# Optimization experiments

Hardware: AMD Instinct MI355X
Metric: run time of the kernel (lower is better)

Reference implementation:

```python
import jax, jax.numpy as jnp
import numpy as np

B, S, D = 4, 8192, 512
WS = 512        # window_size
LB = 1          # look_backward (look_forward = 0, causal)


def setup_inputs() -> dict:
    key = jax.random.key(0)
    k1, k2, k3 = jax.random.split(key, 3)
    text = jax.random.normal(k1, (B, S, D), dtype=jnp.float32)
    audio = jax.random.normal(k2, (B, S, D), dtype=jnp.float32)
    video = jax.random.normal(k3, (B, S, D), dtype=jnp.float32)
    return {"text": text, "audio": audio, "video": video}


def _local_attention(q, k, v, ws=WS, lb=LB):
    # q, k, v: [b, n, d]; sliding-window causal attention, each query window
    # attends to its own window plus `lb` previous windows.
    b, n, d = q.shape
    w = n // ws
    scale = d ** -0.5
    qw = q.reshape(b, w, ws, d) * scale
    kw = k.reshape(b, w, ws, d)
    vw = v.reshape(b, w, ws, d)

    def look_around(x):
        # pad lb windows of zeros at the front, gather lb+1 shifted views
        padded = jnp.pad(x, ((0, 0), (lb, 0), (0, 0), (0, 0)))
        return jnp.concatenate([padded[:, i:i + w] for i in range(lb + 1)], axis=2)

    kk = look_around(kw)  # [b, w, (lb+1)*ws, d]
    vv = look_around(vw)

    # absolute positions for causal + padding mask
    t = jnp.arange(n).reshape(w, ws)                        # query positions [w, ws]
    tk = jnp.pad(t, ((lb, 0), (0, 0)), constant_values=-1)  # pad windows get -1
    bq_k = jnp.concatenate([tk[i:i + w] for i in range(lb + 1)], axis=1)  # [w, (lb+1)*ws]
    mask = (t[:, :, None] >= bq_k[:, None, :]) & (bq_k[:, None, :] >= 0)  # [w, ws, (lb+1)*ws]

    sim = jnp.einsum('bwid,bwjd->bwij', qw, kk)             # [b, w, ws, (lb+1)*ws]
    sim = jnp.where(mask[None], sim, jnp.finfo(sim.dtype).min)
    attn = jax.nn.softmax(sim, axis=-1)
    out = jnp.einsum('bwij,bwjd->bwid', attn, vv)
    return out.reshape(b, n, d)


def reference(text, audio, video):
    # GATSBlock.forward: x = self.local_attn(text, audio, video)
    # i.e. q = text, k = audio, v = video (modalities pre-projected to [b, n, d])
    return _local_attention(text, audio, video)
```

## Files before the change

### kernel.cpp

```cpp
#include <hip/hip_runtime.h>
#include <hip/hip_bf16.h>

#define S_ 8192
#define D_ 512
#define WSZ 512
#define QBLK 128
#define KBLK 64
#define ATT_THREADS 512
#define PPSTRIDE 4352
#define ATT_LDS (131072 + 4 * PPSTRIDE)

using bf16x8 = __attribute__((ext_vector_type(8))) __bf16;
using f32x4  = __attribute__((ext_vector_type(4))) float;
using f32x16 = __attribute__((ext_vector_type(16))) float;

#define GLDS(gp, lp) __builtin_amdgcn_global_load_lds( \
    (const __attribute__((address_space(1))) void*)(gp), \
    (__attribute__((address_space(3))) void*)(lp), 16, 0, 0)

__global__ __launch_bounds__(256) void cvt_k(const float* __restrict__ in,
                                             ushort* __restrict__ out) {
    const int bid = blockIdx.x;
    const int j = bid & 7, t = (bid >> 3) & 255, b = bid >> 11;
    const int u = j * 256 + threadIdx.x;
    const int c = u >> 7, row = (u >> 2) & 31, h = u & 3;
    const float* src = in + ((size_t)(b * S_ + t * 32 + row)) * D_ + c * 32 + h * 8;
    float4 a0 = *(const float4*)(src);
    float4 a1 = *(const float4*)(src + 4);
    bf16x8 o;
    o[0] = (__bf16)a0.x; o[1] = (__bf16)a0.y; o[2] = (__bf16)a0.z; o[3] = (__bf16)a0.w;
    o[4] = (__bf16)a1.x; o[5] = (__bf16)a1.y; o[6] = (__bf16)a1.z; o[7] = (__bf16)a1.w;
    *(bf16x8*)(out + (size_t)(b * 256 + t) * 16384 + u * 8) = o;
}

__global__ __launch_bounds__(256) void tr_v(const float* __restrict__ V,
                                            char* __restrict__ Vt) {
    __shared__ float tile[64][68];
    const int bid = blockIdx.x;
    const int d0 = (bid & 7) * 64;
    const int s0 = ((bid >> 3) & 127) * 64;
    const int b  = bid >> 10;
    const int t  = threadIdx.x;
    {
        const int sl = t >> 2, cg = (t & 3) * 16;
        const float* src = V + ((size_t)b * S_ + s0 + sl) * D_ + d0 + cg;
        #pragma unroll
        for (int j = 0; j < 4; ++j)
            *(float4*)&tile[sl][cg + j * 4] = *(const float4*)(src + j * 4);
    }
    __syncthreads();
    {
        const int dl = t >> 2, sg = (t & 3) * 16;
        const int d  = d0 + dl;
        const int tt = (s0 + sg) >> 5;
        const int kk = (s0 + sg) & 31;
        bf16x8 o0, o1;
        #pragma unroll
        for (int j = 0; j < 8; ++j) {
            o0[j] = (__bf16)tile[sg + j][dl];
            o1[j] = (__bf16)tile[sg + 8 + j][dl];
        }
        char* base = Vt + (size_t)(b * 256 + tt) * 32768 +
                     (d >> 5) * 2048 + (d & 31) * 16;
        *(bf16x8*)(base + (kk >> 4) * 1024)       = o0;
        *(bf16x8*)(base + (kk >> 4) * 1024 + 512) = o1;
    }
}

__global__ __launch_bounds__(ATT_THREADS, 2) void gats_attn(
    const float* __restrict__ Qg, const char* __restrict__ Kbg,
    const char* __restrict__ Vtg, float* __restrict__ Og)
{
    extern __shared__ char smem[];
    char* Vsh = smem + 65536;
    const int tid  = threadIdx.x;
    const int lane = tid & 63;
    const int wv   = tid >> 6;
    const int h    = lane >> 4;
    const int lq   = lane & 15;
    const int hh   = lane >> 5;
    const int l31  = lane & 31;
    const int u    = wv & 1;
    const int pr   = wv >> 1;
    char* Pp = smem + 131072 + pr * PPSTRIDE;
    char* Pf = Pp + 4096;
    const int laneK = lq * 64 + h * 16;

    const int bid = blockIdx.x;
    const int r2  = bid >> 3;
    const int w   = (bid & 7) * 2 + (r2 & 1);
    const int b   = (r2 >> 1) & 3;
    const int y   = r2 >> 3;
    const int qbase    = w * WSZ + y * QBLK;
    const int pairbase = qbase + pr * 32;
    const int wqbase   = qbase + wv * 16;

    const float* Qp  = Qg  + (size_t)b * S_ * D_;
    const char*  Kbp = Kbg + (size_t)b * 256 * 32768;
    const char*  Vtp = Vtg + (size_t)b * 256 * 32768;
    float*       Op  = Og  + (size_t)b * S_ * D_;

    const float scale = 0.044194173824159216f;
    const float L2E   = 1.44269504088896f;

    bf16x8 qf[16];
    {
        const int qrow = wqbase + lq;
        const float* qsrc = Qp + (size_t)qrow * D_ + h * 8;
        #pragma unroll
        for (int c = 0; c < 16; ++c) {
            float4 a0 = *(const float4*)(qsrc + c * 32);
            float4 a1 = *(const float4*)(qsrc + c * 32 + 4);
            bf16x8 q;
            q[0] = (__bf16)(a0.x * scale); q[1] = (__bf16)(a0.y * scale);
            q[2] = (__bf16)(a0.z * scale); q[3] = (__bf16)(a0.w * scale);
            q[4] = (__bf16)(a1.x * scale); q[5] = (__bf16)(a1.y * scale);
            q[6] = (__bf16)(a1.z * scale); q[7] = (__bf16)(a1.w * scale);
            qf[c] = q;
        }
    }

    f32x16 acc[8];
    #pragma unroll
    for (int dt = 0; dt < 8; ++dt)
        #pragma unroll
        for (int rg = 0; rg < 16; ++rg) acc[dt][rg] = 0.f;
    float m_run = -1e30f, l_run = 0.f;

    const int kstart = (w == 0) ? 0 : (w - 1) * WSZ;
    const int ktend  = qbase + QBLK;

    auto STAGE_K = [&](int kt) {
        const char* ksrc = Kbp + (((size_t)(kt >> 5)) << 15);
        #pragma unroll
        for (int s2 = 0; s2 < 8; ++s2) {
            const int off = wv * 8192 + s2 * 1024;
            GLDS(ksrc + off + lane * 16, smem + off);
        }
    };
    auto STAGE_V = [&](int kt) {
        const char* vsrc = Vtp + (((size_t)(kt >> 5)) << 15);
        #pragma unroll
        for (int s2 = 0; s2 < 8; ++s2) {
            const int off = wv * 8192 + s2 * 1024;
            GLDS(vsrc + off + lane * 16, Vsh + off);
        }
    };

    STAGE_K(kstart);
    STAGE_V(kstart);
    for (int kt = kstart; kt < ktend; kt += KBLK) {
        asm volatile("s_waitcnt vmcnt(0)" ::: "memory");
        __builtin_amdgcn_s_barrier();

        const bool act = (kt <= pairbase + 31);
        f32x4 st[4];

        if (act) {
            __builtin_amdgcn_s_setprio(1);
            #pragma unroll
            for (int g = 0; g < 4; ++g) {
                f32x4 sa = (f32x4){0.f, 0.f, 0.f, 0.f};
                f32x4 sb = (f32x4){0.f, 0.f, 0.f, 0.f};
                #pragma unroll
                for (int c = 0; c < 16; ++c) {
                    const int byte = (g >> 1) * 32768 + c * 2048 + (g & 1) * 1024 + laneK;
                    bf16x8 kf = *(const bf16x8*)(smem + byte);
                    if (c & 1) sb = __builtin_amdgcn_mfma_f32_16x16x32_bf16(kf, qf[c], sb, 0, 0, 0);
                    else       sa = __builtin_amdgcn_mfma_f32_16x16x32_bf16(kf, qf[c], sa, 0, 0, 0);
                }
                st[g] = sa + sb;
            }
            __builtin_amdgcn_s_setprio(0);

            const int qg = wqbase + lq;
            if (kt + 63 > wqbase) {
                #pragma unroll
                for (int g = 0; g < 4; ++g)
                    #pragma unroll
                    for (int r = 0; r < 4; ++r) {
                        const int key = kt + g * 16 + h * 4 + r;
                        if (key > qg) st[g][r] = -1e30f;
                    }
            }

            float own = -1e30f;
            #pragma unroll
            for (int g = 0; g < 4; ++g)
                #pragma unroll
                for (int r = 0; r < 4; ++r) own = fmaxf(own, st[g][r]);
            float tmax = fmaxf(own, __shfl_xor(own, 16));
            tmax = fmaxf(tmax, __shfl_xor(tmax, 32));

            const bool anyneed = __any(tmax > m_run + 8.f);
            float f_val = 1.0f;
            if (anyneed) {
                const float mnew = fmaxf(m_run, tmax);
                f_val = exp2f((m_run - mnew) * L2E);
                m_run = mnew;
                l_run *= f_val;
            }

            float p[4][4];
            float rs = 0.f;
            #pragma unroll
            for (int g = 0; g < 4; ++g)
                #pragma unroll
                for (int r = 0; r < 4; ++r) {
                    const float v = exp2f((st[g][r] - m_run) * L2E);
                    p[g][r] = v;
                    rs += v;
                }
            rs += __shfl_xor(rs, 16);
            rs += __shfl_xor(rs, 32);
            l_run += rs;

            uint cA[4], cB[4];
            #pragma unroll
            for (int g = 0; g < 4; ++g) {
                asm("v_cvt_pk_bf16_f32 %0, %1, %2" : "=v"(cA[g]) : "v"(p[g][0]), "v"(p[g][1]));
                asm("v_cvt_pk_bf16_f32 %0, %1, %2" : "=v"(cB[g]) : "v"(p[g][2]), "v"(p[g][3]));
            }
            const int wbase = (h >> 1) * 512 + (h & 1) * 8 + (u * 16 + lq) * 16;
            #pragma unroll
            for (int g = 0; g < 4; ++g) {
                *(uint*)(Pp + g * 1024 + wbase)     = cA[g];
                *(uint*)(Pp + g * 1024 + wbase + 4) = cB[g];
            }
            if (h == 0)    *(float*)(Pf + (u * 16 + lq) * 4) = f_val;
            if (lane == 0) *(uint*)(Pf + 128 + u * 4) = anyneed ? 1u : 0u;
        }

        asm volatile("s_waitcnt lgkmcnt(0)" ::: "memory");
        __builtin_amdgcn_sched_barrier(0);
        __builtin_amdgcn_s_barrier();

        if (kt + KBLK < ktend) STAGE_K(kt + KBLK);

        if (act) {
            const uint2 fl = *(const uint2*)(Pf + 128);
            if (fl.x | fl.y) {
                f32x4 fr[4];
                #pragma unroll
                for (int i = 0; i < 4; ++i)
                    fr[i] = *(const f32x4*)(Pf + i * 32 + hh * 16);
                #pragma unroll
                for (int dt = 0; dt < 8; ++dt)
                    #pragma unroll
                    for (int rg = 0; rg < 16; ++rg)
                        acc[dt][rg] *= fr[rg >> 2][rg & 3];
            }

            bf16x8 pa[4];
            #pragma unroll
            for (int ks = 0; ks < 4; ++ks)
                pa[ks] = *(const bf16x8*)(Pp + ks * 1024 + hh * 512 + l31 * 16);
            __builtin_amdgcn_s_setprio(1);
            #pragma unroll
            for (int dt = 0; dt < 8; ++dt) {
                #pragma unroll
                for (int ks = 0; ks < 4; ++ks) {
                    const int vb = (ks >> 1) * 32768 + (u * 8 + dt) * 2048 +
                                   (ks & 1) * 1024 + hh * 512 + l31 * 16;
                    bf16x8 vf = *(const bf16x8*)(Vsh + vb);
                    acc[dt] = __builtin_amdgcn_mfma_f32_32x32x16_bf16(pa[ks], vf, acc[dt], 0, 0, 0);
                }
            }
            __builtin_amdgcn_s_setprio(0);
        }
        __builtin_amdgcn_s_barrier();
        if (kt + KBLK < ktend) STAGE_V(kt + KBLK);
    }

    if (h == 0) *(float*)(Pf + (u * 16 + lq) * 4) = l_run;
    asm volatile("s_waitcnt lgkmcnt(0)" ::: "memory");
    __builtin_amdgcn_s_barrier();
    f32x4 iv[4];
    #pragma unroll
    for (int i = 0; i < 4; ++i) {
        f32x4 lv = *(const f32x4*)(Pf + i * 32 + hh * 16);
        iv[i][0] = 1.0f / lv[0]; iv[i][1] = 1.0f / lv[1];
        iv[i][2] = 1.0f / lv[2]; iv[i][3] = 1.0f / lv[3];
    }
    #pragma unroll
    for (int dt = 0; dt < 8; ++dt) {
        const int colb = u * 256 + dt * 32 + l31;
        #pragma unroll
        for (int rg = 0; rg < 16; ++rg) {
            const int row = pairbase + (rg & 3) + 8 * (rg >> 2) + 4 * hh;
            Op[(size_t)row * D_ + colb] = acc[dt][rg] * iv[rg >> 2][rg & 3];
        }
    }
}

#define FB_LDS (32768 + 32768 + 4 * 1024)
__global__ __launch_bounds__(256, 2) void gats_attn_fb(
    const float* __restrict__ Qg, const float* __restrict__ Kg,
    const float* __restrict__ Vg, float* __restrict__ Og)
{
    extern __shared__ char smem[];
    char* Ksh = smem;
    char* Vsh = smem + 32768;
    const int tid  = threadIdx.x;
    const int lane = tid & 63;
    const int wv   = tid >> 6;
    char* Psh = smem + 65536 + wv * 1024;
    const int bid = blockIdx.x;
    const int wh  = bid & 7;
    const int r2  = bid >> 3;
    const int w   = wh * 2 + (r2 & 1);
    const int b   = (r2 >> 1) & 3;
    const int y   = r2 >> 3;
    const int qbase  = w * WSZ + y * 64;
    const int wqbase = qbase + wv * 16;
    const size_t boff = (size_t)b * S_ * D_;
    const float* Qp = Qg + boff; const float* Kp = Kg + boff;
    const float* Vp = Vg + boff; float* Op = Og + boff;
    const float scale = 0.044194173824159216f;
    const float L2E   = 1.44269504088896f;
    bf16x8 qf[16];
    {
        const int qrow = wqbase + (lane & 15);
        const float* qsrc = Qp + (size_t)qrow * D_ + ((lane >> 4) * 8);
        #pragma unroll
        for (int c = 0; c < 16; ++c) {
            float4 a0 = *(const float4*)(qsrc + c * 32);
            float4 a1 = *(const float4*)(qsrc + c * 32 + 4);
            bf16x8 q;
            q[0] = (__bf16)(a0.x * scale); q[1] = (__bf16)(a0.y * scale);
            q[2] = (__bf16)(a0.z * scale); q[3] = (__bf16)(a0.w * scale);
            q[4] = (__bf16)(a1.x * scale); q[5] = (__bf16)(a1.y * scale);
            q[6] = (__bf16)(a1.z * scale); q[7] = (__bf16)(a1.w * scale);
            qf[c] = q;
        }
    }
    f32x4 acc[32];
    #pragma unroll
    for (int i = 0; i < 32; ++i) acc[i] = (f32x4){0.f, 0.f, 0.f, 0.f};
    float m_r[4], l_r[4];
    #pragma unroll
    for (int r = 0; r < 4; ++r) { m_r[r] = -1e30f; l_r[r] = 0.f; }
    const int kstart = (w == 0) ? 0 : (w - 1) * WSZ;
    const int ktend  = qbase + 64;
    for (int kt = kstart; kt < ktend; kt += 32) {
        __syncthreads();
        #pragma unroll
        for (int s = 0; s < 8; ++s) {
            const int row = s * 4 + wv;
            const int dof = lane * 8;
            const float4* src = (const float4*)(Kp + (size_t)(kt + row) * D_ + dof);
            float4 a0 = src[0], a1 = src[1];
            bf16x8 kv;
            kv[0] = (__bf16)a0.x; kv[1] = (__bf16)a0.y; kv[2] = (__bf16)a0.z; kv[3] = (__bf16)a0.w;
            kv[4] = (__bf16)a1.x; kv[5] = (__bf16)a1.y; kv[6] = (__bf16)a1.z; kv[7] = (__bf16)a1.w;
            const int byte = row * 1024 + ((dof * 2) ^ ((row & 7) << 4));
            *(bf16x8*)(Ksh + byte) = kv;
        }
        #pragma unroll
        for (int hh2 = 0; hh2 < 2; ++hh2) {
            const int d = tid + hh2 * 256;
            #pragma unroll
            for (int it = 0; it < 4; ++it) {
                float vvv[8];
                #pragma unroll
                for (int j = 0; j < 8; ++j)
                    vvv[j] = Vp[(size_t)(kt + it * 8 + j) * D_ + d];
                bf16x8 vb;
                #pragma unroll
                for (int j = 0; j < 8; ++j) vb[j] = (__bf16)vvv[j];
                const int byte = d * 64 + ((it * 16) ^ (((d >> 1) & 3) << 4));
                *(bf16x8*)(Vsh + byte) = vb;
            }
        }
        __syncthreads();
        if (kt > wqbase + 15) continue;
        f32x4 sacc[2];
        #pragma unroll
        for (int g = 0; g < 2; ++g) {
            f32x4 s = (f32x4){0.f, 0.f, 0.f, 0.f};
            const int keyrow = g * 16 + (lane & 15);
            #pragma unroll
            for (int c = 0; c < 16; ++c) {
                const int byte = keyrow * 1024 +
                                 ((c * 64 + (lane >> 4) * 16) ^ ((keyrow & 7) << 4));
                bf16x8 kf = *(const bf16x8*)(Ksh + byte);
                s = __builtin_amdgcn_mfma_f32_16x16x32_bf16(qf[c], kf, s, 0, 0, 0);
            }
            sacc[g] = s;
        }
        #pragma unroll
        for (int g = 0; g < 2; ++g) {
            if (kt + g * 16 + 15 > wqbase) {
                const int kg = kt + g * 16 + (lane & 15);
                #pragma unroll
                for (int r = 0; r < 4; ++r) {
                    const int qrow = wqbase + (lane >> 4) * 4 + r;
                    if (kg > qrow) sacc[g][r] = -1e30f;
                }
            }
        }
        float tmax[4];
        #pragma unroll
        for (int r = 0; r < 4; ++r) {
            float v = fmaxf(sacc[0][r], sacc[1][r]);
            #pragma unroll
            for (int off = 8; off >= 1; off >>= 1)
                v = fmaxf(v, __shfl_xor(v, off));
            tmax[r] = v;
        }
        bool need = false;
        #pragma unroll
        for (int r = 0; r < 4; ++r) need |= (tmax[r] > m_r[r] + 8.f);
        if (__any(need)) {
            #pragma unroll
            for (int r = 0; r < 4; ++r) {
                const float mnew = fmaxf(m_r[r], tmax[r]);
                const float f = exp2f((m_r[r] - mnew) * L2E);
                m_r[r] = mnew; l_r[r] *= f;
                #pragma unroll
                for (int dc = 0; dc < 32; ++dc) acc[dc][r] *= f;
            }
        }
        float rsum[4] = {0.f, 0.f, 0.f, 0.f};
        #pragma unroll
        for (int g = 0; g < 2; ++g) {
            #pragma unroll
            for (int r = 0; r < 4; ++r) {
                const float p = exp2f((sacc[g][r] - m_r[r]) * L2E);
                rsum[r] += p;
                const int prow = (lane >> 4) * 4 + r;
                const int byte = prow * 64 +
                                 ((g * 32 + (lane & 15) * 2) ^ (((prow >> 1) & 3) << 4));
                *(__bf16*)(Psh + byte) = (__bf16)p;
            }
        }
        #pragma unroll
        for (int r = 0; r < 4; ++r) {
            float v = rsum[r];
            #pragma unroll
            for (int off = 8; off >= 1; off >>= 1)
                v += __shfl_xor(v, off);
            l_r[r] += v;
        }
        {
            const int prow  = lane & 15;
            const int pbyte = prow * 64 +
                              (((lane >> 4) * 16) ^ (((prow >> 1) & 3) << 4));
            bf16x8 pa = *(const bf16x8*)(Psh + pbyte);
            #pragma unroll
            for (int dc = 0; dc < 32; ++dc) {
                const int d = dc * 16 + (lane & 15);
                const int vbyte = d * 64 +
                                  (((lane >> 4) * 16) ^ (((d >> 1) & 3) << 4));
                bf16x8 vf = *(const bf16x8*)(Vsh + vbyte);
                acc[dc] = __builtin_amdgcn_mfma_f32_16x16x32_bf16(pa, vf, acc[dc], 0, 0, 0);
            }
        }
    }
    float inv[4];
    #pragma unroll
    for (int r = 0; r < 4; ++r) inv[r] = 1.0f / l_r[r];
    #pragma unroll
    for (int dc = 0; dc < 32; ++dc) {
        #pragma unroll
        for (int r = 0; r < 4; ++r) {
            const int row = wqbase + (lane >> 4) * 4 + r;
            const int col = dc * 16 + (lane & 15);
            Op[(size_t)row * D_ + col] = acc[dc][r] * inv[r];
        }
    }
}

extern "C" void kernel_launch(void* const* d_in, const int* in_sizes, int n_in,
                              void* d_out, int out_size, void* d_ws, size_t ws_size,
                              hipStream_t stream) {
    const float* q = (const float*)d_in[0];
    const float* k = (const float*)d_in[1];
    const float* v = (const float*)d_in[2];
    float* o = (float*)d_out;

    const size_t elems = (size_t)4 * S_ * D_ * 4;
    const size_t need  = elems * 2 * 2;
    if (ws_size >= need) {
        char* kb = (char*)d_ws;
        char* vt = (char*)d_ws + elems * 2;
        cvt_k<<<dim3(8192), dim3(256), 0, stream>>>(k, (ushort*)kb);
        tr_v <<<dim3(4096), dim3(256), 0, stream>>>(v, vt);
        hipFuncSetAttribute((const void*)gats_attn,
                            hipFuncAttributeMaxDynamicSharedMemorySize, ATT_LDS);
        gats_attn<<<dim3(256), dim3(ATT_THREADS), ATT_LDS, stream>>>(q, kb, vt, o);
    } else {
        hipFuncSetAttribute((const void*)gats_attn_fb,
                            hipFuncAttributeMaxDynamicSharedMemorySize, FB_LDS);
        gats_attn_fb<<<dim3(512), dim3(256), FB_LDS, stream>>>(q, k, v, o);
    }
}
```

Baseline: 149.9 us.

## Split head dim across waves with cross-wave score reduction and smaller tiles

Restructures the attention kernel so each block handles 32 queries with 4 waves. Each wave owns a quarter of the head dimension for both QK^T and PV, and partial scores are summed across waves through LDS. Key blocks shrink to 16 and the grid grows from 256 to 1024 blocks with smaller LDS, aiming for more occupancy and better load balance across CUs. The cost is an extra barrier per key step, LDS traffic for partial scores, and far more K/V tile reloads per query, which lowers data reuse.

```diff
diff --git a/kernel.cpp b/kernel.cpp
--- a/kernel.cpp
+++ b/kernel.cpp
@@ -4,11 +4,9 @@
 #define S_ 8192
 #define D_ 512
 #define WSZ 512
-#define QBLK 128
-#define KBLK 64
-#define ATT_THREADS 512
-#define PPSTRIDE 4352
-#define ATT_LDS (131072 + 4 * PPSTRIDE)
+#define KBLK 16
+#define ATT_THREADS 256
+#define ATT_LDS 42240
 
 using bf16x8 = __attribute__((ext_vector_type(8))) __bf16;
 using f32x4  = __attribute__((ext_vector_type(4))) float;
@@ -67,33 +65,30 @@
     }
 }
 
-__global__ __launch_bounds__(ATT_THREADS, 2) void gats_attn(
+__global__ __launch_bounds__(ATT_THREADS, 3) void gats_attn(
     const float* __restrict__ Qg, const char* __restrict__ Kbg,
     const char* __restrict__ Vtg, float* __restrict__ Og)
 {
     extern __shared__ char smem[];
-    char* Vsh = smem + 65536;
+    char* Ksh = smem;
+    char* Vsh = smem + 16384;
+    char* Ex  = smem + 32768;
+    char* Pp  = smem + 40960;
+    char* Pf  = smem + 41984;
     const int tid  = threadIdx.x;
     const int lane = tid & 63;
-    const int wv   = tid >> 6;
+    const int v    = tid >> 6;
     const int h    = lane >> 4;
     const int lq   = lane & 15;
     const int hh   = lane >> 5;
     const int l31  = lane & 31;
-    const int u    = wv & 1;
-    const int pr   = wv >> 1;
-    char* Pp = smem + 131072 + pr * PPSTRIDE;
-    char* Pf = Pp + 4096;
-    const int laneK = lq * 64 + h * 16;
 
     const int bid = blockIdx.x;
     const int r2  = bid >> 3;
     const int w   = (bid & 7) * 2 + (r2 & 1);
     const int b   = (r2 >> 1) & 3;
-    const int y   = r2 >> 3;
-    const int qbase    = w * WSZ + y * QBLK;
-    const int pairbase = qbase + pr * 32;
-    const int wqbase   = qbase + wv * 16;
+    const int yq  = r2 >> 3;
+    const int qbase = w * WSZ + yq * 32;
 
     const float* Qp  = Qg  + (size_t)b * S_ * D_;
     const char*  Kbp = Kbg + (size_t)b * 256 * 32768;
@@ -103,47 +98,48 @@
     const float scale = 0.044194173824159216f;
     const float L2E   = 1.44269504088896f;
 
-    bf16x8 qf[16];
-    {
-        const int qrow = wqbase + lq;
-        const float* qsrc = Qp + (size_t)qrow * D_ + h * 8;
-        #pragma unroll
-        for (int c = 0; c < 16; ++c) {
-            float4 a0 = *(const float4*)(qsrc + c * 32);
-            float4 a1 = *(const float4*)(qsrc + c * 32 + 4);
+    bf16x8 qf[2][4];
+    #pragma unroll
+    for (int qh = 0; qh < 2; ++qh) {
+        const int qrow = qbase + qh * 16 + lq;
+        const float* qsrc = Qp + (size_t)qrow * D_ + v * 128 + h * 8;
+        #pragma unroll
+        for (int cc = 0; cc < 4; ++cc) {
+            float4 a0 = *(const float4*)(qsrc + cc * 32);
+            float4 a1 = *(const float4*)(qsrc + cc * 32 + 4);
             bf16x8 q;
             q[0] = (__bf16)(a0.x * scale); q[1] = (__bf16)(a0.y * scale);
             q[2] = (__bf16)(a0.z * scale); q[3] = (__bf16)(a0.w * scale);
             q[4] = (__bf16)(a1.x * scale); q[5] = (__bf16)(a1.y * scale);
             q[6] = (__bf16)(a1.z * scale); q[7] = (__bf16)(a1.w * scale);
-            qf[c] = q;
-        }
-    }
-
-    f32x16 acc[8];
-    #pragma unroll
-    for (int dt = 0; dt < 8; ++dt)
-        #pragma unroll
-        for (int rg = 0; rg < 16; ++rg) acc[dt][rg] = 0.f;
+            qf[qh][cc] = q;
+        }
+    }
+
+    f32x16 acc[4];
+    #pragma unroll
+    for (int ch = 0; ch < 4; ++ch)
+        #pragma unroll
+        for (int rg = 0; rg < 16; ++rg) acc[ch][rg] = 0.f;
     float m_run = -1e30f, l_run = 0.f;
 
     const int kstart = (w == 0) ? 0 : (w - 1) * WSZ;
-    const int ktend  = qbase + QBLK;
+    const int ktend  = qbase + 32;
 
     auto STAGE_K = [&](int kt) {
-        const char* ksrc = Kbp + (((size_t)(kt >> 5)) << 15);
-        #pragma unroll
-        for (int s2 = 0; s2 < 8; ++s2) {
-            const int off = wv * 8192 + s2 * 1024;
-            GLDS(ksrc + off + lane * 16, smem + off);
+        const char* base = Kbp + ((size_t)(kt >> 5) << 15) + ((kt >> 4) & 1) * 1024;
+        #pragma unroll
+        for (int cc = 0; cc < 4; ++cc) {
+            const int c = v * 4 + cc;
+            GLDS(base + c * 2048 + lane * 16, Ksh + c * 1024 + lane * 16);
         }
     };
     auto STAGE_V = [&](int kt) {
-        const char* vsrc = Vtp + (((size_t)(kt >> 5)) << 15);
-        #pragma unroll
-        for (int s2 = 0; s2 < 8; ++s2) {
-            const int off = wv * 8192 + s2 * 1024;
-            GLDS(vsrc + off + lane * 16, Vsh + off);
+        const char* base = Vtp + ((size_t)(kt >> 5) << 15) + ((kt >> 4) & 1) * 1024;
+        #pragma unroll
+        for (int cc = 0; cc < 4; ++cc) {
+            const int d32 = v * 4 + cc;
+            GLDS(base + d32 * 2048 + lane * 16, Vsh + d32 * 1024 + lane * 16);
         }
     };
 
@@ -153,42 +149,46 @@
         asm volatile("s_waitcnt vmcnt(0)" ::: "memory");
         __builtin_amdgcn_s_barrier();
 
-        const bool act = (kt <= pairbase + 31);
-        f32x4 st[4];
-
+        const bool act = (kt <= qbase + 31);
+
+        f32x4 stp0 = (f32x4){0.f,0.f,0.f,0.f};
+        f32x4 stp1 = (f32x4){0.f,0.f,0.f,0.f};
         if (act) {
             __builtin_amdgcn_s_setprio(1);
             #pragma unroll
-            for (int g = 0; g < 4; ++g) {
-                f32x4 sa = (f32x4){0.f, 0.f, 0.f, 0.f};
-                f32x4 sb = (f32x4){0.f, 0.f, 0.f, 0.f};
-                #pragma unroll
-                for (int c = 0; c < 16; ++c) {
-                    const int byte = (g >> 1) * 32768 + c * 2048 + (g & 1) * 1024 + laneK;
-                    bf16x8 kf = *(const bf16x8*)(smem + byte);
-                    if (c & 1) sb = __builtin_amdgcn_mfma_f32_16x16x32_bf16(kf, qf[c], sb, 0, 0, 0);
-                    else       sa = __builtin_amdgcn_mfma_f32_16x16x32_bf16(kf, qf[c], sa, 0, 0, 0);
+            for (int cc = 0; cc < 4; ++cc) {
+                const int byte = (v * 4 + cc) * 1024 + lq * 64 + h * 16;
+                bf16x8 kf = *(const bf16x8*)(Ksh + byte);
+                stp0 = __builtin_amdgcn_mfma_f32_16x16x32_bf16(kf, qf[0][cc], stp0, 0, 0, 0);
+                stp1 = __builtin_amdgcn_mfma_f32_16x16x32_bf16(kf, qf[1][cc], stp1, 0, 0, 0);
+            }
+            __builtin_amdgcn_s_setprio(0);
+            *(f32x4*)(Ex + v * 2048 + lane * 16)        = stp0;
+            *(f32x4*)(Ex + v * 2048 + 1024 + lane * 16) = stp1;
+        }
+
+        asm volatile("s_waitcnt lgkmcnt(0)" ::: "memory");
+        __builtin_amdgcn_sched_barrier(0);
+        __builtin_amdgcn_s_barrier();
+
+        if (kt + KBLK < ktend) STAGE_K(kt + KBLK);
+
+        if (act && v < 2) {
+            f32x4 st = (v == 0) ? stp0 : stp1;
+            #pragma unroll
+            for (int vp = 0; vp < 4; ++vp) {
+                if (vp != v)
+                    st += *(const f32x4*)(Ex + vp * 2048 + v * 1024 + lane * 16);
+            }
+            const int qg = qbase + v * 16 + lq;
+            if (kt + 15 > qbase) {
+                #pragma unroll
+                for (int r = 0; r < 4; ++r) {
+                    const int key = kt + h * 4 + r;
+                    if (key > qg) st[r] = -1e30f;
                 }
-                st[g] = sa + sb;
-            }
-            __builtin_amdgcn_s_setprio(0);
-
-            const int qg = wqbase + lq;
-            if (kt + 63 > wqbase) {
-                #pragma unroll
-                for (int g = 0; g < 4; ++g)
-                    #pragma unroll
-                    for (int r = 0; r < 4; ++r) {
-                        const int key = kt + g * 16 + h * 4 + r;
-                        if (key > qg) st[g][r] = -1e30f;
-                    }
-            }
-
-            float own = -1e30f;
-            #pragma unroll
-            for (int g = 0; g < 4; ++g)
-                #pragma unroll
-                for (int r = 0; r < 4; ++r) own = fmaxf(own, st[g][r]);
+            }
+            float own = fmaxf(fmaxf(st[0], st[1]), fmaxf(st[2], st[3]));
             float tmax = fmaxf(own, __shfl_xor(own, 16));
             tmax = fmaxf(tmax, __shfl_xor(tmax, 32));
 
@@ -200,42 +200,28 @@
                 m_run = mnew;
                 l_run *= f_val;
             }
-
-            float p[4][4];
-            float rs = 0.f;
-            #pragma unroll
-            for (int g = 0; g < 4; ++g)
-                #pragma unroll
-                for (int r = 0; r < 4; ++r) {
-                    const float v = exp2f((st[g][r] - m_run) * L2E);
-                    p[g][r] = v;
-                    rs += v;
-                }
+            const float p0 = exp2f((st[0] - m_run) * L2E);
+            const float p1 = exp2f((st[1] - m_run) * L2E);
+            const float p2 = exp2f((st[2] - m_run) * L2E);
+            const float p3 = exp2f((st[3] - m_run) * L2E);
+            float rs = p0 + p1 + p2 + p3;
             rs += __shfl_xor(rs, 16);
             rs += __shfl_xor(rs, 32);
             l_run += rs;
 
-            uint cA[4], cB[4];
-            #pragma unroll
-            for (int g = 0; g < 4; ++g) {
-                asm("v_cvt_pk_bf16_f32 %0, %1, %2" : "=v"(cA[g]) : "v"(p[g][0]), "v"(p[g][1]));
-                asm("v_cvt_pk_bf16_f32 %0, %1, %2" : "=v"(cB[g]) : "v"(p[g][2]), "v"(p[g][3]));
-            }
-            const int wbase = (h >> 1) * 512 + (h & 1) * 8 + (u * 16 + lq) * 16;
-            #pragma unroll
-            for (int g = 0; g < 4; ++g) {
-                *(uint*)(Pp + g * 1024 + wbase)     = cA[g];
-                *(uint*)(Pp + g * 1024 + wbase + 4) = cB[g];
-            }
-            if (h == 0)    *(float*)(Pf + (u * 16 + lq) * 4) = f_val;
-            if (lane == 0) *(uint*)(Pf + 128 + u * 4) = anyneed ? 1u : 0u;
+            uint c0, c1;
+            asm("v_cvt_pk_bf16_f32 %0, %1, %2" : "=v"(c0) : "v"(p0), "v"(p1));
+            asm("v_cvt_pk_bf16_f32 %0, %1, %2" : "=v"(c1) : "v"(p2), "v"(p3));
+            const int wbase = (h >> 1) * 512 + (h & 1) * 8 + (v * 16 + lq) * 16;
+            *(uint*)(Pp + wbase)     = c0;
+            *(uint*)(Pp + wbase + 4) = c1;
+            if (h == 0)    *(float*)(Pf + (v * 16 + lq) * 4) = f_val;
+            if (lane == 0) *(uint*)(Pf + 128 + v * 4) = anyneed ? 1u : 0u;
         }
 
         asm volatile("s_waitcnt lgkmcnt(0)" ::: "memory");
         __builtin_amdgcn_sched_barrier(0);
         __builtin_amdgcn_s_barrier();
-
-        if (kt + KBLK < ktend) STAGE_K(kt + KBLK);
 
         if (act) {
             const uint2 fl = *(const uint2*)(Pf + 128);
@@ -245,26 +231,18 @@
                 for (int i = 0; i < 4; ++i)
                     fr[i] = *(const f32x4*)(Pf + i * 32 + hh * 16);
                 #pragma unroll
-                for (int dt = 0; dt < 8; ++dt)
+                for (int ch = 0; ch < 4; ++ch)
                     #pragma unroll
                     for (int rg = 0; rg < 16; ++rg)
-                        acc[dt][rg] *= fr[rg >> 2][rg & 3];
-            }
-
-            bf16x8 pa[4];
-            #pragma unroll
-            for (int ks = 0; ks < 4; ++ks)
-                pa[ks] = *(const bf16x8*)(Pp + ks * 1024 + hh * 512 + l31 * 16);
+                        acc[ch][rg] *= fr[rg >> 2][rg & 3];
+            }
+            bf16x8 pa = *(const bf16x8*)(Pp + hh * 512 + l31 * 16);
             __builtin_amdgcn_s_setprio(1);
             #pragma unroll
-            for (int dt = 0; dt < 8; ++dt) {
-                #pragma unroll
-                for (int ks = 0; ks < 4; ++ks) {
-                    const int vb = (ks >> 1) * 32768 + (u * 8 + dt) * 2048 +
-                                   (ks & 1) * 1024 + hh * 512 + l31 * 16;
-                    bf16x8 vf = *(const bf16x8*)(Vsh + vb);
-                    acc[dt] = __builtin_amdgcn_mfma_f32_32x32x16_bf16(pa[ks], vf, acc[dt], 0, 0, 0);
-                }
+            for (int ch = 0; ch < 4; ++ch) {
+                const int vb = (v * 4 + ch) * 1024 + hh * 512 + l31 * 16;
+                bf16x8 vf = *(const bf16x8*)(Vsh + vb);
+                acc[ch] = __builtin_amdgcn_mfma_f32_32x32x16_bf16(pa, vf, acc[ch], 0, 0, 0);
             }
             __builtin_amdgcn_s_setprio(0);
         }
@@ -272,7 +250,7 @@
         if (kt + KBLK < ktend) STAGE_V(kt + KBLK);
     }
 
-    if (h == 0) *(float*)(Pf + (u * 16 + lq) * 4) = l_run;
+    if (v < 2 && h == 0) *(float*)(Pf + (v * 16 + lq) * 4) = l_run;
     asm volatile("s_waitcnt lgkmcnt(0)" ::: "memory");
     __builtin_amdgcn_s_barrier();
     f32x4 iv[4];
@@ -283,12 +261,12 @@
         iv[i][2] = 1.0f / lv[2]; iv[i][3] = 1.0f / lv[3];
     }
     #pragma unroll
-    for (int dt = 0; dt < 8; ++dt) {
-        const int colb = u * 256 + dt * 32 + l31;
+    for (int ch = 0; ch < 4; ++ch) {
+        const int colb = v * 128 + ch * 32 + l31;
         #pragma unroll
         for (int rg = 0; rg < 16; ++rg) {
-            const int row = pairbase + (rg & 3) + 8 * (rg >> 2) + 4 * hh;
-            Op[(size_t)row * D_ + colb] = acc[dt][rg] * iv[rg >> 2][rg & 3];
+            const int row = qbase + (rg & 3) + 8 * (rg >> 2) + 4 * hh;
+            Op[(size_t)row * D_ + colb] = acc[ch][rg] * iv[rg >> 2][rg & 3];
         }
     }
 }
@@ -402,11 +380,11 @@
         float tmax[4];
         #pragma unroll
         for (int r = 0; r < 4; ++r) {
-            float v = fmaxf(sacc[0][r], sacc[1][r]);
+            float vv = fmaxf(sacc[0][r], sacc[1][r]);
             #pragma unroll
             for (int off = 8; off >= 1; off >>= 1)
-                v = fmaxf(v, __shfl_xor(v, off));
-            tmax[r] = v;
+                vv = fmaxf(vv, __shfl_xor(vv, off));
+            tmax[r] = vv;
         }
         bool need = false;
         #pragma unroll
@@ -436,11 +414,11 @@
         }
         #pragma unroll
         for (int r = 0; r < 4; ++r) {
-            float v = rsum[r];
+            float vv = rsum[r];
             #pragma unroll
             for (int off = 8; off >= 1; off >>= 1)
-                v += __shfl_xor(v, off);
-            l_r[r] += v;
+                vv += __shfl_xor(vv, off);
+            l_r[r] += vv;
         }
         {
             const int prow  = lane & 15;
@@ -488,7 +466,7 @@
         tr_v <<<dim3(4096), dim3(256), 0, stream>>>(v, vt);
         hipFuncSetAttribute((const void*)gats_attn,
                             hipFuncAttributeMaxDynamicSharedMemorySize, ATT_LDS);
-        gats_attn<<<dim3(256), dim3(ATT_THREADS), ATT_LDS, stream>>>(q, kb, vt, o);
+        gats_attn<<<dim3(1024), dim3(ATT_THREADS), ATT_LDS, stream>>>(q, kb, vt, o);
     } else {
         hipFuncSetAttribute((const void*)gats_attn_fb,
                             hipFuncAttributeMaxDynamicSharedMemorySize, FB_LDS);
```

Result: slower. 211.0 us (+40.7%).
